# Kernel optimization log

Hardware: AMD Instinct MI355X
Metric: run time of the kernel (lower is better)

## Reference

```python
import jax, jax.numpy as jnp
from jax import lax
import numpy as np

EPS = 1e-06


def _box_filter(x, radius):
    # Depthwise box mean with zero padding (matches F.conv2d padding=radius),
    # implemented separably: O(r) per pixel instead of O(r^2).
    C = x.shape[1]
    k = 2 * radius + 1
    dn = ('NCHW', 'OIHW', 'NCHW')
    kern_h = jnp.ones((C, 1, k, 1), x.dtype)
    kern_w = jnp.ones((C, 1, 1, k), x.dtype) / (k * k)
    y = lax.conv_general_dilated(x, kern_h, (1, 1), [(radius, radius), (0, 0)],
                                 feature_group_count=C, dimension_numbers=dn)
    return lax.conv_general_dilated(y, kern_w, (1, 1), [(0, 0), (radius, radius)],
                                    feature_group_count=C, dimension_numbers=dn)


def setup_inputs() -> dict:
    key = jax.random.key(0)
    k1, k2 = jax.random.split(key)
    I = jax.random.uniform(k1, (8, 1, 1024, 1024), dtype=jnp.float32)
    p = jax.random.uniform(k2, (8, 3, 1024, 1024), dtype=jnp.float32)
    return {"I": I, "p": p, "radius": 3}


def reference(I, p, radius):
    mean_I = _box_filter(I, radius)            # (B,1,H,W)
    mean_p = _box_filter(p, radius)            # (B,3,H,W)
    mean_Ip = _box_filter(I * p, radius)
    mean_II = _box_filter(I * I, radius)
    cov_Ip = mean_Ip - mean_I * mean_p
    var_I = mean_II - mean_I * mean_I
    a = cov_Ip / (var_I + EPS)
    b = mean_p - a * mean_I
    mean_a = _box_filter(a, radius)
    mean_b = _box_filter(b, radius)
    q = mean_a * I + mean_b
    return jnp.clip(q, 0.0, 1.0)
```

## Files before the change

kernel.cpp:

```cpp
#include <hip/hip_runtime.h>


#define TPB   128
#define OUTW  116
#define SEGH  64
#define HW    1024
#define GW    134
#define EPSF  1e-6f
#define INV49 (1.0f/49.0f)

struct GFState {
    float csI, csII, csp0, csp1, csp2, csq0, csq1, csq2;
    float hrI[8], hrII[8], hrp0[8], hrp1[8], hrp2[8], hrq0[8], hrq1[8], hrq2[8];
    float c2a0, c2b0, c2a1, c2b1, c2a2, c2b2;
    float h2a0[8], h2b0[8], h2a1[8], h2b1[8], h2a2[8], h2b2[8];
    float ha[4][3], hb[4][3];
    float4 cur[4];
    float  Iq[4], IqN[4];
};

template<int JB>
__device__ __forceinline__ void halfStep(
    GFState& S, int j0, int Y0, int x_in, bool xok, int xc, int tid,
    const float* __restrict__ Ip, const float* __restrict__ P0,
    const float* __restrict__ P1, const float* __restrict__ P2,
    float* __restrict__ Q0, float* __restrict__ Q1, float* __restrict__ Q2,
    float4 (*rawbuf)[GW], float4 (*abA)[GW], float2 (*abB)[GW],
    bool dostore, bool dopref)
{
    __syncthreads();

    #pragma unroll
    for (int u = 0; u < 4; ++u) {
        rawbuf[(JB+u)&3][tid+3] = S.cur[u];
        const int w = (JB+u+1)&3;
        abA[w][tid+3] = make_float4(S.ha[u][0], S.hb[u][0], S.ha[u][1], S.hb[u][1]);
        abB[w][tid+3] = make_float2(S.ha[u][2], S.hb[u][2]);
    }
    __syncthreads();

    if (dopref) {
        #pragma unroll
        for (int u = 0; u < 4; ++u) {
            int y = Y0 + j0 + 4 + u;
            bool ok = xok && ((unsigned)y < HW);
            int yy = min(max(y, 0), HW-1);
            size_t off = (size_t)yy*HW + xc;
            float a0 = Ip[off], a1 = P0[off], a2 = P1[off], a3 = P2[off];
            float4 v;
            v.x = ok ? a0 : 0.f; v.y = ok ? a1 : 0.f;
            v.z = ok ? a2 : 0.f; v.w = ok ? a3 : 0.f;
            S.cur[u] = v;
        }
        #pragma unroll
        for (int u = 0; u < 4; ++u) {
            int o = Y0 + j0 - 6 + u;
            bool ok = xok && ((unsigned)o < HW);
            int oo = min(max(o, 0), HW-1);
            float v = Ip[(size_t)oo*HW + xc];
            S.IqN[u] = ok ? v : 0.f;
        }
    }

    #pragma unroll
    for (int u = 0; u < 4; ++u) {
        const int lslot  = (JB+u)&3;
        const int lslotw = (JB+u+1)&3;
        const int rslot  = (JB+u)&7;
        const int rslotw = (JB+u+1)&7;
        const int rslot2 = (JB+u+2)&7;
        const int y = Y0 + j0 + u;

        float hI=0,hII=0,hp0=0,hp1=0,hp2=0,hq0=0,hq1=0,hq2=0;
        #pragma unroll
        for (int d = 0; d < 7; ++d) {
            float4 t = rawbuf[lslot][tid+d];
            hI  += t.x; hII = fmaf(t.x, t.x, hII);
            hp0 += t.y; hq0 = fmaf(t.x, t.y, hq0);
            hp1 += t.z; hq1 = fmaf(t.x, t.z, hq1);
            hp2 += t.w; hq2 = fmaf(t.x, t.w, hq2);
        }
        S.csI  += hI  - S.hrI [rslotw]; S.hrI [rslot] = hI;
        S.csII += hII - S.hrII[rslotw]; S.hrII[rslot] = hII;
        S.csp0 += hp0 - S.hrp0[rslotw]; S.hrp0[rslot] = hp0;
        S.csp1 += hp1 - S.hrp1[rslotw]; S.hrp1[rslot] = hp1;
        S.csp2 += hp2 - S.hrp2[rslotw]; S.hrp2[rslot] = hp2;
        S.csq0 += hq0 - S.hrq0[rslotw]; S.hrq0[rslot] = hq0;
        S.csq1 += hq1 - S.hrq1[rslotw]; S.hrq1[rslot] = hq1;
        S.csq2 += hq2 - S.hrq2[rslotw]; S.hrq2[rslot] = hq2;

        {
            float mi_ = S.csI*INV49, mii = S.csII*INV49;
            float rv  = __builtin_amdgcn_rcpf(mii - mi_*mi_ + EPSF);
            bool abok = xok && ((unsigned)(y-3) < HW);
            float mp, mq, a, b;
            mp = S.csp0*INV49; mq = S.csq0*INV49;
            a = (mq - mi_*mp)*rv; b = fmaf(-a, mi_, mp);
            S.ha[u][0] = abok ? a : 0.f; S.hb[u][0] = abok ? b : 0.f;
            mp = S.csp1*INV49; mq = S.csq1*INV49;
            a = (mq - mi_*mp)*rv; b = fmaf(-a, mi_, mp);
            S.ha[u][1] = abok ? a : 0.f; S.hb[u][1] = abok ? b : 0.f;
            mp = S.csp2*INV49; mq = S.csq2*INV49;
            a = (mq - mi_*mp)*rv; b = fmaf(-a, mi_, mp);
            S.ha[u][2] = abok ? a : 0.f; S.hb[u][2] = abok ? b : 0.f;
        }

        float sa0=0,sb0=0,sa1=0,sb1=0,sa2=0,sb2=0;
        #pragma unroll
        for (int d = 0; d < 7; ++d) {
            float4 A = abA[lslotw][tid+d];
            float2 B = abB[lslotw][tid+d];
            sa0 += A.x; sb0 += A.y; sa1 += A.z; sb1 += A.w;
            sa2 += B.x; sb2 += B.y;
        }
        S.c2a0 += sa0 - S.h2a0[rslot2]; S.h2a0[rslotw] = sa0;
        S.c2b0 += sb0 - S.h2b0[rslot2]; S.h2b0[rslotw] = sb0;
        S.c2a1 += sa1 - S.h2a1[rslot2]; S.h2a1[rslotw] = sa1;
        S.c2b1 += sb1 - S.h2b1[rslot2]; S.h2b1[rslotw] = sb1;
        S.c2a2 += sa2 - S.h2a2[rslot2]; S.h2a2[rslotw] = sa2;
        S.c2b2 += sb2 - S.h2b2[rslot2]; S.h2b2[rslotw] = sb2;

        if (dostore) {
            int o = y - 10;
            float Io = S.Iq[u];
            bool sok = (tid >= 6) && (tid < 122) && (x_in < HW);
            size_t ooff = (size_t)o*HW + x_in;
            float q;
            q = fmaf(S.c2a0*INV49, Io, S.c2b0*INV49);
            q = fminf(fmaxf(q, 0.f), 1.f); if (sok) Q0[ooff] = q;
            q = fmaf(S.c2a1*INV49, Io, S.c2b1*INV49);
            q = fminf(fmaxf(q, 0.f), 1.f); if (sok) Q1[ooff] = q;
            q = fmaf(S.c2a2*INV49, Io, S.c2b2*INV49);
            q = fminf(fmaxf(q, 0.f), 1.f); if (sok) Q2[ooff] = q;
        }
    }

    #pragma unroll
    for (int u = 0; u < 4; ++u) S.Iq[u] = S.IqN[u];
}

__global__ __launch_bounds__(TPB, 1) void gf_kernel(
    const float* __restrict__ I, const float* __restrict__ P,
    float* __restrict__ Q)
{
    __shared__ float4 rawbuf[4][GW];
    __shared__ float4 abA[4][GW];
    __shared__ float2 abB[4][GW];

    const int s   = blockIdx.x;
    const int seg = blockIdx.y;
    const int b   = blockIdx.z;
    const int tid = threadIdx.x;

    const int X0   = s*OUTW - 6;
    const int Y0   = seg*SEGH - 6;
    const int x_in = X0 + tid;
    const bool xok = (unsigned)x_in < HW;
    const int  xc  = min(max(x_in, 0), HW-1);

    const float* Ip = I + (size_t)b*HW*HW;
    const float* P0 = P + ((size_t)b*3 + 0)*HW*HW;
    const float* P1 = P + ((size_t)b*3 + 1)*HW*HW;
    const float* P2 = P + ((size_t)b*3 + 2)*HW*HW;
    float* Q0 = Q + ((size_t)b*3 + 0)*HW*HW;
    float* Q1 = Q + ((size_t)b*3 + 1)*HW*HW;
    float* Q2 = Q + ((size_t)b*3 + 2)*HW*HW;

    GFState S;
    S.csI=S.csII=S.csp0=S.csp1=S.csp2=S.csq0=S.csq1=S.csq2=0.f;
    S.c2a0=S.c2b0=S.c2a1=S.c2b1=S.c2a2=S.c2b2=0.f;
    #pragma unroll
    for (int i = 0; i < 8; ++i) {
        S.hrI[i]=S.hrII[i]=S.hrp0[i]=S.hrp1[i]=S.hrp2[i]=0.f;
        S.hrq0[i]=S.hrq1[i]=S.hrq2[i]=0.f;
        S.h2a0[i]=S.h2b0[i]=S.h2a1[i]=S.h2b1[i]=S.h2a2[i]=S.h2b2[i]=0.f;
    }
    #pragma unroll
    for (int u = 0; u < 4; ++u) {
        S.ha[u][0]=S.ha[u][1]=S.ha[u][2]=0.f;
        S.hb[u][0]=S.hb[u][1]=S.hb[u][2]=0.f;
        S.Iq[u]=S.IqN[u]=0.f;
    }
    #pragma unroll
    for (int u = 0; u < 4; ++u) {
        int y = Y0 + u;
        bool ok = xok && ((unsigned)y < HW);
        int yy = min(max(y, 0), HW-1);
        size_t off = (size_t)yy*HW + xc;
        float a0 = Ip[off], a1 = P0[off], a2 = P1[off], a3 = P2[off];
        float4 v;
        v.x = ok ? a0 : 0.f; v.y = ok ? a1 : 0.f;
        v.z = ok ? a2 : 0.f; v.w = ok ? a3 : 0.f;
        S.cur[u] = v;
    }

    for (int m = 0; m < 10; ++m) {
        int j0 = m*8;
        halfStep<0>(S, j0,   Y0, x_in, xok, xc, tid, Ip, P0, P1, P2,
                    Q0, Q1, Q2, rawbuf, abA, abB,
                    (j0   >= 16), true);
        halfStep<4>(S, j0+4, Y0, x_in, xok, xc, tid, Ip, P0, P1, P2,
                    Q0, Q1, Q2, rawbuf, abA, abB,
                    (j0+4 >= 16), (j0+4) < 76);
    }
}

extern "C" void kernel_launch(void* const* d_in, const int* in_sizes, int n_in,
                              void* d_out, int out_size, void* d_ws, size_t ws_size,
                              hipStream_t stream) {
    const float* I = (const float*)d_in[0];
    const float* P = (const float*)d_in[1];
    float* Q = (float*)d_out;

    dim3 grid(9, 16, 8);
    gf_kernel<<<grid, TPB, 0, stream>>>(I, P, Q);
}
```

Measured before the change: 314.3 us.

## Reorder box filter to vertical-first running sums and drop I reload

Each thread now keeps vertical running sums of I, I², p and I·p in registers and publishes those column sums to shared memory, so the 7-tap horizontal pass runs over column sums instead of over raw pixels. The second filter stage does the same with vertical running sums of a and b. The guide value needed for the output is read from a register ring, so the extra global reload of I is gone, and the pipeline latency drops, removing one outer iteration. Launch bounds rise to allow three blocks per CU, and the shared buffers are zero-initialised. Running sums built by add and subtract can drift slightly in float precision, and the larger shared footprint and register pressure could limit occupancy.

```diff
diff --git a/kernel.cpp b/kernel.cpp
--- a/kernel.cpp
+++ b/kernel.cpp
@@ -10,142 +10,131 @@
 #define INV49 (1.0f/49.0f)
 
 struct GFState {
-    float csI, csII, csp0, csp1, csp2, csq0, csq1, csq2;
-    float hrI[8], hrII[8], hrp0[8], hrp1[8], hrp2[8], hrq0[8], hrq1[8], hrq2[8];
-    float c2a0, c2b0, c2a1, c2b1, c2a2, c2b2;
-    float h2a0[8], h2b0[8], h2a1[8], h2b1[8], h2a2[8], h2b2[8];
-    float ha[4][3], hb[4][3];
+    float4 rr[8];
+    float ra0[8], rb0[8], ra1[8], rb1[8], ra2[8], rb2[8];
+    float sI, sII, sp0, sp1, sp2, sq0, sq1, sq2;
+    float t6a0, t6b0, t6a1, t6b1, t6a2, t6b2;
     float4 cur[4];
-    float  Iq[4], IqN[4];
 };
 
 template<int JB>
 __device__ __forceinline__ void halfStep(
-    GFState& S, int j0, int Y0, int x_in, bool xok, int xc, int tid,
+    GFState& S, int j0, int Yb, int x_in, bool xok, int xc, int tid,
     const float* __restrict__ Ip, const float* __restrict__ P0,
     const float* __restrict__ P1, const float* __restrict__ P2,
     float* __restrict__ Q0, float* __restrict__ Q1, float* __restrict__ Q2,
-    float4 (*rawbuf)[GW], float4 (*abA)[GW], float2 (*abB)[GW],
+    float4 (*cs8A)[GW], float4 (*cs8B)[GW],
+    float4 (*cs6A)[GW], float2 (*cs6B)[GW],
     bool dostore, bool dopref)
 {
+    float Io[4];
+    #pragma unroll
+    for (int u = 0; u < 4; ++u) Io[u] = S.rr[(JB+u+2)&7].x;
+
+    #pragma unroll
+    for (int u = 0; u < 4; ++u) {
+        const float4 c = S.cur[u];
+        const float4 o = S.rr[(JB+u+1)&7];
+        S.sI  += c.x - o.x;
+        S.sII += c.x*c.x - o.x*o.x;
+        S.sp0 += c.y - o.y;  S.sq0 += c.x*c.y - o.x*o.y;
+        S.sp1 += c.z - o.z;  S.sq1 += c.x*c.z - o.x*o.z;
+        S.sp2 += c.w - o.w;  S.sq2 += c.x*c.w - o.x*o.w;
+        S.rr[(JB+u)&7] = c;
+        cs8A[(JB+u)&3][tid+3] = make_float4(S.sI,  S.sII, S.sp0, S.sp1);
+        cs8B[(JB+u)&3][tid+3] = make_float4(S.sp2, S.sq0, S.sq1, S.sq2);
+    }
     __syncthreads();
 
     #pragma unroll
     for (int u = 0; u < 4; ++u) {
-        rawbuf[(JB+u)&3][tid+3] = S.cur[u];
-        const int w = (JB+u+1)&3;
-        abA[w][tid+3] = make_float4(S.ha[u][0], S.hb[u][0], S.ha[u][1], S.hb[u][1]);
-        abB[w][tid+3] = make_float2(S.ha[u][2], S.hb[u][2]);
+        const int ls = (JB+u)&3;
+        float4 A = make_float4(0.f,0.f,0.f,0.f);
+        float4 B = make_float4(0.f,0.f,0.f,0.f);
+        #pragma unroll
+        for (int d = 0; d < 7; ++d) {
+            float4 a = cs8A[ls][tid+d];
+            float4 b = cs8B[ls][tid+d];
+            A.x += a.x; A.y += a.y; A.z += a.z; A.w += a.w;
+            B.x += b.x; B.y += b.y; B.z += b.z; B.w += b.w;
+        }
+        const int  yc   = Yb + j0 + u - 3;
+        const bool abok = xok && ((unsigned)yc < HW);
+        const float mi  = A.x*INV49, mii = A.y*INV49;
+        const float rv  = __builtin_amdgcn_rcpf(mii - mi*mi + EPSF);
+        float a0,b0,a1,b1,a2,b2, mp, mq, a, b;
+        mp = A.z*INV49; mq = B.y*INV49;
+        a = (mq - mi*mp)*rv; b = fmaf(-a, mi, mp);
+        a0 = abok ? a : 0.f; b0 = abok ? b : 0.f;
+        mp = A.w*INV49; mq = B.z*INV49;
+        a = (mq - mi*mp)*rv; b = fmaf(-a, mi, mp);
+        a1 = abok ? a : 0.f; b1 = abok ? b : 0.f;
+        mp = B.x*INV49; mq = B.w*INV49;
+        a = (mq - mi*mp)*rv; b = fmaf(-a, mi, mp);
+        a2 = abok ? a : 0.f; b2 = abok ? b : 0.f;
+
+        const int as = (JB+u)&7, al = (JB+u+1)&7;
+        S.t6a0 += a0 - S.ra0[al]; S.ra0[as] = a0;
+        S.t6b0 += b0 - S.rb0[al]; S.rb0[as] = b0;
+        S.t6a1 += a1 - S.ra1[al]; S.ra1[as] = a1;
+        S.t6b1 += b1 - S.rb1[al]; S.rb1[as] = b1;
+        S.t6a2 += a2 - S.ra2[al]; S.ra2[as] = a2;
+        S.t6b2 += b2 - S.rb2[al]; S.rb2[as] = b2;
+        cs6A[ls][tid+3] = make_float4(S.t6a0, S.t6b0, S.t6a1, S.t6b1);
+        cs6B[ls][tid+3] = make_float2(S.t6a2, S.t6b2);
     }
     __syncthreads();
 
     if (dopref) {
         #pragma unroll
         for (int u = 0; u < 4; ++u) {
-            int y = Y0 + j0 + 4 + u;
-            bool ok = xok && ((unsigned)y < HW);
-            int yy = min(max(y, 0), HW-1);
-            size_t off = (size_t)yy*HW + xc;
-            float a0 = Ip[off], a1 = P0[off], a2 = P1[off], a3 = P2[off];
+            const int y  = Yb + j0 + 4 + u;
+            const bool ok = xok && ((unsigned)y < HW);
+            const int yy = min(max(y, 0), HW-1);
+            const size_t off = (size_t)yy*HW + xc;
+            float v0 = Ip[off], v1 = P0[off], v2 = P1[off], v3 = P2[off];
             float4 v;
-            v.x = ok ? a0 : 0.f; v.y = ok ? a1 : 0.f;
-            v.z = ok ? a2 : 0.f; v.w = ok ? a3 : 0.f;
+            v.x = ok ? v0 : 0.f; v.y = ok ? v1 : 0.f;
+            v.z = ok ? v2 : 0.f; v.w = ok ? v3 : 0.f;
             S.cur[u] = v;
         }
+    }
+
+    if (dostore) {
+        const bool sok = (tid >= 6) && (tid < 122) && (x_in < HW);
         #pragma unroll
         for (int u = 0; u < 4; ++u) {
-            int o = Y0 + j0 - 6 + u;
-            bool ok = xok && ((unsigned)o < HW);
-            int oo = min(max(o, 0), HW-1);
-            float v = Ip[(size_t)oo*HW + xc];
-            S.IqN[u] = ok ? v : 0.f;
-        }
-    }
-
-    #pragma unroll
-    for (int u = 0; u < 4; ++u) {
-        const int lslot  = (JB+u)&3;
-        const int lslotw = (JB+u+1)&3;
-        const int rslot  = (JB+u)&7;
-        const int rslotw = (JB+u+1)&7;
-        const int rslot2 = (JB+u+2)&7;
-        const int y = Y0 + j0 + u;
-
-        float hI=0,hII=0,hp0=0,hp1=0,hp2=0,hq0=0,hq1=0,hq2=0;
-        #pragma unroll
-        for (int d = 0; d < 7; ++d) {
-            float4 t = rawbuf[lslot][tid+d];
-            hI  += t.x; hII = fmaf(t.x, t.x, hII);
-            hp0 += t.y; hq0 = fmaf(t.x, t.y, hq0);
-            hp1 += t.z; hq1 = fmaf(t.x, t.z, hq1);
-            hp2 += t.w; hq2 = fmaf(t.x, t.w, hq2);
-        }
-        S.csI  += hI  - S.hrI [rslotw]; S.hrI [rslot] = hI;
-        S.csII += hII - S.hrII[rslotw]; S.hrII[rslot] = hII;
-        S.csp0 += hp0 - S.hrp0[rslotw]; S.hrp0[rslot] = hp0;
-        S.csp1 += hp1 - S.hrp1[rslotw]; S.hrp1[rslot] = hp1;
-        S.csp2 += hp2 - S.hrp2[rslotw]; S.hrp2[rslot] = hp2;
-        S.csq0 += hq0 - S.hrq0[rslotw]; S.hrq0[rslot] = hq0;
-        S.csq1 += hq1 - S.hrq1[rslotw]; S.hrq1[rslot] = hq1;
-        S.csq2 += hq2 - S.hrq2[rslotw]; S.hrq2[rslot] = hq2;
-
-        {
-            float mi_ = S.csI*INV49, mii = S.csII*INV49;
-            float rv  = __builtin_amdgcn_rcpf(mii - mi_*mi_ + EPSF);
-            bool abok = xok && ((unsigned)(y-3) < HW);
-            float mp, mq, a, b;
-            mp = S.csp0*INV49; mq = S.csq0*INV49;
-            a = (mq - mi_*mp)*rv; b = fmaf(-a, mi_, mp);
-            S.ha[u][0] = abok ? a : 0.f; S.hb[u][0] = abok ? b : 0.f;
-            mp = S.csp1*INV49; mq = S.csq1*INV49;
-            a = (mq - mi_*mp)*rv; b = fmaf(-a, mi_, mp);
-            S.ha[u][1] = abok ? a : 0.f; S.hb[u][1] = abok ? b : 0.f;
-            mp = S.csp2*INV49; mq = S.csq2*INV49;
-            a = (mq - mi_*mp)*rv; b = fmaf(-a, mi_, mp);
-            S.ha[u][2] = abok ? a : 0.f; S.hb[u][2] = abok ? b : 0.f;
-        }
-
-        float sa0=0,sb0=0,sa1=0,sb1=0,sa2=0,sb2=0;
-        #pragma unroll
-        for (int d = 0; d < 7; ++d) {
-            float4 A = abA[lslotw][tid+d];
-            float2 B = abB[lslotw][tid+d];
-            sa0 += A.x; sb0 += A.y; sa1 += A.z; sb1 += A.w;
-            sa2 += B.x; sb2 += B.y;
-        }
-        S.c2a0 += sa0 - S.h2a0[rslot2]; S.h2a0[rslotw] = sa0;
-        S.c2b0 += sb0 - S.h2b0[rslot2]; S.h2b0[rslotw] = sb0;
-        S.c2a1 += sa1 - S.h2a1[rslot2]; S.h2a1[rslotw] = sa1;
-        S.c2b1 += sb1 - S.h2b1[rslot2]; S.h2b1[rslotw] = sb1;
-        S.c2a2 += sa2 - S.h2a2[rslot2]; S.h2a2[rslotw] = sa2;
-        S.c2b2 += sb2 - S.h2b2[rslot2]; S.h2b2[rslotw] = sb2;
-
-        if (dostore) {
-            int o = y - 10;
-            float Io = S.Iq[u];
-            bool sok = (tid >= 6) && (tid < 122) && (x_in < HW);
-            size_t ooff = (size_t)o*HW + x_in;
+            const int ls = (JB+u)&3;
+            float4 A6 = make_float4(0.f,0.f,0.f,0.f);
+            float2 B6 = make_float2(0.f,0.f);
+            #pragma unroll
+            for (int d = 0; d < 7; ++d) {
+                float4 a = cs6A[ls][tid+d];
+                float2 b = cs6B[ls][tid+d];
+                A6.x += a.x; A6.y += a.y; A6.z += a.z; A6.w += a.w;
+                B6.x += b.x; B6.y += b.y;
+            }
+            const int o = Yb + j0 + u - 6;
+            const size_t ooff = (size_t)o*HW + x_in;
             float q;
-            q = fmaf(S.c2a0*INV49, Io, S.c2b0*INV49);
+            q = fmaf(A6.x*INV49, Io[u], A6.y*INV49);
             q = fminf(fmaxf(q, 0.f), 1.f); if (sok) Q0[ooff] = q;
-            q = fmaf(S.c2a1*INV49, Io, S.c2b1*INV49);
+            q = fmaf(A6.z*INV49, Io[u], A6.w*INV49);
             q = fminf(fmaxf(q, 0.f), 1.f); if (sok) Q1[ooff] = q;
-            q = fmaf(S.c2a2*INV49, Io, S.c2b2*INV49);
+            q = fmaf(B6.x*INV49, Io[u], B6.y*INV49);
             q = fminf(fmaxf(q, 0.f), 1.f); if (sok) Q2[ooff] = q;
         }
     }
-
-    #pragma unroll
-    for (int u = 0; u < 4; ++u) S.Iq[u] = S.IqN[u];
 }
 
-__global__ __launch_bounds__(TPB, 1) void gf_kernel(
+__global__ __launch_bounds__(TPB, 3) void gf_kernel(
     const float* __restrict__ I, const float* __restrict__ P,
     float* __restrict__ Q)
 {
-    __shared__ float4 rawbuf[4][GW];
-    __shared__ float4 abA[4][GW];
-    __shared__ float2 abB[4][GW];
+    __shared__ float4 cs8A[4][GW];
+    __shared__ float4 cs8B[4][GW];
+    __shared__ float4 cs6A[4][GW];
+    __shared__ float2 cs6B[4][GW];
 
     const int s   = blockIdx.x;
     const int seg = blockIdx.y;
@@ -153,7 +142,7 @@
     const int tid = threadIdx.x;
 
     const int X0   = s*OUTW - 6;
-    const int Y0   = seg*SEGH - 6;
+    const int Yb   = seg*SEGH - 6;
     const int x_in = X0 + tid;
     const bool xok = (unsigned)x_in < HW;
     const int  xc  = min(max(x_in, 0), HW-1);
@@ -166,43 +155,53 @@
     float* Q1 = Q + ((size_t)b*3 + 1)*HW*HW;
     float* Q2 = Q + ((size_t)b*3 + 2)*HW*HW;
 
+    {
+        float4* zA = (float4*)cs8A;
+        float4* zB = (float4*)cs8B;
+        float4* zC = (float4*)cs6A;
+        float2* zD = (float2*)cs6B;
+        const float4 z4 = make_float4(0.f,0.f,0.f,0.f);
+        const float2 z2 = make_float2(0.f,0.f);
+        for (int i = tid; i < 4*GW; i += TPB) {
+            zA[i] = z4; zB[i] = z4; zC[i] = z4; zD[i] = z2;
+        }
+    }
+
     GFState S;
-    S.csI=S.csII=S.csp0=S.csp1=S.csp2=S.csq0=S.csq1=S.csq2=0.f;
-    S.c2a0=S.c2b0=S.c2a1=S.c2b1=S.c2a2=S.c2b2=0.f;
+    S.sI=S.sII=S.sp0=S.sp1=S.sp2=S.sq0=S.sq1=S.sq2=0.f;
+    S.t6a0=S.t6b0=S.t6a1=S.t6b1=S.t6a2=S.t6b2=0.f;
     #pragma unroll
     for (int i = 0; i < 8; ++i) {
-        S.hrI[i]=S.hrII[i]=S.hrp0[i]=S.hrp1[i]=S.hrp2[i]=0.f;
-        S.hrq0[i]=S.hrq1[i]=S.hrq2[i]=0.f;
-        S.h2a0[i]=S.h2b0[i]=S.h2a1[i]=S.h2b1[i]=S.h2a2[i]=S.h2b2[i]=0.f;
+        S.rr[i] = make_float4(0.f,0.f,0.f,0.f);
+        S.ra0[i]=S.rb0[i]=S.ra1[i]=S.rb1[i]=S.ra2[i]=S.rb2[i]=0.f;
     }
     #pragma unroll
     for (int u = 0; u < 4; ++u) {
-        S.ha[u][0]=S.ha[u][1]=S.ha[u][2]=0.f;
-        S.hb[u][0]=S.hb[u][1]=S.hb[u][2]=0.f;
-        S.Iq[u]=S.IqN[u]=0.f;
-    }
-    #pragma unroll
-    for (int u = 0; u < 4; ++u) {
-        int y = Y0 + u;
-        bool ok = xok && ((unsigned)y < HW);
-        int yy = min(max(y, 0), HW-1);
-        size_t off = (size_t)yy*HW + xc;
-        float a0 = Ip[off], a1 = P0[off], a2 = P1[off], a3 = P2[off];
+        const int y = Yb + u;
+        const bool ok = xok && ((unsigned)y < HW);
+        const int yy = min(max(y, 0), HW-1);
+        const size_t off = (size_t)yy*HW + xc;
+        float v0 = Ip[off], v1 = P0[off], v2 = P1[off], v3 = P2[off];
         float4 v;
-        v.x = ok ? a0 : 0.f; v.y = ok ? a1 : 0.f;
-        v.z = ok ? a2 : 0.f; v.w = ok ? a3 : 0.f;
+        v.x = ok ? v0 : 0.f; v.y = ok ? v1 : 0.f;
+        v.z = ok ? v2 : 0.f; v.w = ok ? v3 : 0.f;
         S.cur[u] = v;
     }
 
-    for (int m = 0; m < 10; ++m) {
-        int j0 = m*8;
-        halfStep<0>(S, j0,   Y0, x_in, xok, xc, tid, Ip, P0, P1, P2,
-                    Q0, Q1, Q2, rawbuf, abA, abB,
-                    (j0   >= 16), true);
-        halfStep<4>(S, j0+4, Y0, x_in, xok, xc, tid, Ip, P0, P1, P2,
-                    Q0, Q1, Q2, rawbuf, abA, abB,
-                    (j0+4 >= 16), (j0+4) < 76);
-    }
+    __syncthreads();
+
+    for (int m = 0; m < 9; ++m) {
+        const int j0 = m*8;
+        halfStep<0>(S, j0,   Yb, x_in, xok, xc, tid, Ip, P0, P1, P2,
+                    Q0, Q1, Q2, cs8A, cs8B, cs6A, cs6B,
+                    (j0   >= 12), true);
+        halfStep<4>(S, j0+4, Yb, x_in, xok, xc, tid, Ip, P0, P1, P2,
+                    Q0, Q1, Q2, cs8A, cs8B, cs6A, cs6B,
+                    (j0+4 >= 12), true);
+    }
+    halfStep<0>(S, 72, Yb, x_in, xok, xc, tid, Ip, P0, P1, P2,
+                Q0, Q1, Q2, cs8A, cs8B, cs6A, cs6B,
+                true, false);
 }
 
 extern "C" void kernel_launch(void* const* d_in, const int* in_sizes, int n_in,
```

Result: faster. 294.4 us (-6.3%).
